# Kernel optimization log

Measured on AMD Instinct MI355X. Metric: run time of the kernel, lower is better.

The kernel has to match this reference:

```python
import jax, jax.numpy as jnp
import numpy as np

# Sparse 3D conv (stride-2 downsample) followed by the matching SparseInverseConv3d,
# implemented as rulebook-style gather-GEMM-scatter. Output coordinates of the
# inverse conv are exactly the input coordinates (spconv indice_key semantics).
SPATIAL = (41, 400, 352)          # (D, H, W) voxel grid
K, S, P, DIL = 3, 2, 1, 1          # kernel, stride, padding, dilation
IN_CH, OUT_CH = 32, 64
N_VOX = 120000
BATCH = 2

# static kernel offsets [27, 3]
OFFSETS = np.stack(np.meshgrid(np.arange(K), np.arange(K), np.arange(K), indexing='ij'), -1).reshape(-1, 3)
OUT_SHAPE = tuple((s + 2 * P - DIL * (K - 1) - 1) // S + 1 for s in SPATIAL)  # (21, 200, 176)


def setup_inputs() -> dict:
    key = jax.random.key(0)
    kf, kw1, kw2, kb, kz, ky, kx = jax.random.split(key, 7)
    features = jax.random.normal(kf, (N_VOX, IN_CH), jnp.float32)
    coors = jnp.stack([
        jax.random.randint(kb, (N_VOX,), 0, BATCH),
        jax.random.randint(kz, (N_VOX,), 0, SPATIAL[0]),
        jax.random.randint(ky, (N_VOX,), 0, SPATIAL[1]),
        jax.random.randint(kx, (N_VOX,), 0, SPATIAL[2]),
    ], axis=1).astype(jnp.int32)
    W1 = jax.random.normal(kw1, (K ** 3, IN_CH, OUT_CH), jnp.float32) * (1.0 / np.sqrt(K ** 3 * IN_CH))
    W2 = jax.random.normal(kw2, (K ** 3, OUT_CH, IN_CH), jnp.float32) * (1.0 / np.sqrt(K ** 3 * OUT_CH))
    return {"features": features, "coors": coors, "W1": W1, "W2": W2, "batch_size": BATCH}


def _rulebook(coors, batch_size):
    """Per kernel-offset linear output index + validity. lin == G marks invalid (dump slot)."""
    Dz, Hy, Wx = OUT_SHAPE
    G = batch_size * Dz * Hy * Wx
    b = coors[:, 0]
    c = coors[:, 1:]                                    # [N, 3]
    out_shape = jnp.asarray(OUT_SHAPE, jnp.int32)
    lins, valids = [], []
    for kv in range(K ** 3):
        off = jnp.asarray(OFFSETS[kv], jnp.int32)
        oc = c + P - DIL * off                          # numerator of output coord
        oq = oc // S
        valid = ((oc % S == 0) & (oq >= 0) & (oq < out_shape)).all(-1)
        lin = ((b * Dz + oq[:, 0]) * Hy + oq[:, 1]) * Wx + oq[:, 2]
        lins.append(jnp.where(valid, lin, G))
        valids.append(valid)
    return lins, G


def _spconv_forward(features, coors, W1, W2, batch_size):
    lins, G = _rulebook(coors, batch_size)
    # ---- SparseConv3d: gather(all inputs) -> GEMM per offset -> scatter-add to downsampled grid
    grid = jnp.zeros((G + 1, OUT_CH), features.dtype)   # last row = dump slot
    for kv in range(K ** 3):
        grid = grid.at[lins[kv]].add(features @ W1[kv])
    grid = grid.at[G].set(0.0)                          # clear dump slot -> invalid gathers read 0
    # ---- SparseInverseConv3d: transposed rulebook, output sites = original input coords
    out = jnp.zeros((features.shape[0], IN_CH), features.dtype)
    for kv in range(K ** 3):
        out = out + grid[lins[kv]] @ W2[kv]
    return out


def reference(features, coors, W1, W2, batch_size):
    return _spconv_forward(features, coors, W1, W2, int(batch_size))
```

## Files before the change

### kernel.cpp

```cpp
#include <hip/hip_runtime.h>
#include <stdint.h>


#define N_VOX 120000
#define IC 32
#define OC 64
#define NKV 27
#define DZ 21
#define HY 200
#define WX 176
#define TBL_BITS 20
#define TBL_SIZE (1 << TBL_BITS)
#define TBL_MASK (TBL_SIZE - 1)
#define MAXROWS 480000
#define VPW 128
#define VPBLK (VPW * 4)

#define OFF_KEYS 0
#define OFF_VALS 4194304
#define OFF_CNT 8388608
#define OFF_ROWS 8388864
#define OFF_FEATB 21348864
#define OFF_W2T 29028864
#define OFF_GRID 29139456
#define WS_NEEDED (OFF_GRID + (size_t)MAXROWS * OC * 2)

typedef __attribute__((ext_vector_type(8))) short short8;
typedef __attribute__((ext_vector_type(4))) float f32x4;

__device__ __forceinline__ uint32_t hash_lin(int lin) {
    return ((uint32_t)lin * 2654435761u) >> (32 - TBL_BITS);
}

__device__ __forceinline__ void atomAddF32(float* p, float v) {
    unsafeAtomicAdd(p, v);
}

__device__ __forceinline__ void atomPkBf16(uint16_t* p, uint32_t v) {
    asm volatile("global_atomic_pk_add_bf16 %0, %1, off" :: "v"(p), "v"(v) : "memory");
}

__device__ __forceinline__ uint32_t pk_bf16(float a, float b) {
    uint32_t x = __float_as_uint(a), y = __float_as_uint(b);
    x = (x + 0x7fffu + ((x >> 16) & 1u)) >> 16;
    y = (y + 0x7fffu + ((y >> 16) & 1u)) >> 16;
    return x | (y << 16);
}
__device__ __forceinline__ uint16_t f2bf(float a) {
    uint32_t x = __float_as_uint(a);
    return (uint16_t)((x + 0x7fffu + ((x >> 16) & 1u)) >> 16);
}

__device__ __forceinline__ float bf_lo(uint32_t u) { return __uint_as_float(u << 16); }
__device__ __forceinline__ float bf_hi(uint32_t u) { return __uint_as_float(u & 0xffff0000u); }

__global__ void k_init(int* keys, int* counter,
                       const float2* __restrict__ feat2, uint32_t* featb,
                       const float* __restrict__ W2, uint16_t* w2t) {
    int i = blockIdx.x * blockDim.x + threadIdx.x;
    int stride = gridDim.x * blockDim.x;
    for (int j = i; j < TBL_SIZE; j += stride) keys[j] = -1;
    for (int j = i; j < N_VOX * IC / 2; j += stride) {
        float2 f = feat2[j];
        featb[j] = pk_bf16(f.x, f.y);
    }
    for (int j = i; j < NKV * OC * IC; j += stride) {
        int kv = j >> 11, o = (j >> 5) & 63, c = j & 31;
        w2t[(kv << 11) + (c << 6) + o] = f2bf(W2[j]);
    }
    if (i == 0) *counter = 0;
}

__global__ void k_build(const int* __restrict__ coors, int* keys, int* rows) {
    int v = blockIdx.x * blockDim.x + threadIdx.x;
    if (v >= N_VOX) return;
    int b = coors[v * 4 + 0];
    int z = coors[v * 4 + 1];
    int y = coors[v * 4 + 2];
    int x = coors[v * 4 + 3];
#pragma unroll
    for (int kv = 0; kv < NKV; ++kv) {
        int oz = kv / 9, oy = (kv / 3) % 3, ox = kv % 3;
        int az = z + 1 - oz, ay = y + 1 - oy, ax = x + 1 - ox;
        int slot = -1;
        bool valid = (az >= 0) && !(az & 1) && ((az >> 1) < DZ) &&
                     (ay >= 0) && !(ay & 1) && ((ay >> 1) < HY) &&
                     (ax >= 0) && !(ax & 1) && ((ax >> 1) < WX);
        if (valid) {
            int lin = ((b * DZ + (az >> 1)) * HY + (ay >> 1)) * WX + (ax >> 1);
            uint32_t h = hash_lin(lin);
            for (;;) {
                int k = atomicCAS(&keys[h], -1, lin);
                if (k == -1 || k == lin) { slot = (int)h; break; }
                h = (h + 1) & TBL_MASK;
            }
        }
        rows[kv * N_VOX + v] = slot;
    }
}

__global__ __launch_bounds__(256) void k_assign(const int* __restrict__ keys,
                                                int* __restrict__ vals,
                                                int* counter,
                                                float4* __restrict__ grid4) {
    const int t = threadIdx.x;
    const int s0 = blockIdx.x * 2048 + t * 8;
    const int4 a = ((const int4*)(keys + s0))[0];
    const int4 b = ((const int4*)(keys + s0))[1];
    int k[8] = {a.x, a.y, a.z, a.w, b.x, b.y, b.z, b.w};
    int c = 0;
#pragma unroll
    for (int i = 0; i < 8; ++i) c += (k[i] != -1);

    __shared__ int sc[256];
    __shared__ int base;
    sc[t] = c;
    __syncthreads();
#pragma unroll
    for (int d = 1; d < 256; d <<= 1) {
        int y = (t >= d) ? sc[t - d] : 0;
        __syncthreads();
        sc[t] += y;
        __syncthreads();
    }
    if (t == 255) base = atomicAdd(counter, sc[255]);
    __syncthreads();
    const int total = sc[255];
    int r = base + sc[t] - c;
#pragma unroll
    for (int i = 0; i < 8; ++i) {
        if (k[i] != -1) { vals[s0 + i] = (r < MAXROWS) ? r : -1; ++r; }
    }
    int zs = min(base, MAXROWS), ze = min(base + total, MAXROWS);
    float4 zz = {0.f, 0.f, 0.f, 0.f};
    for (int i = zs * 8 + t; i < ze * 8; i += 256) grid4[i] = zz;
}

__global__ void k_rows_fix(int* rows, const int* __restrict__ vals) {
    int i = blockIdx.x * blockDim.x + threadIdx.x;
    if (i >= NKV * N_VOX) return;
    int s = rows[i];
    rows[i] = (s >= 0) ? vals[s] : -1;
}

__device__ __forceinline__ int compact_pairs(const int* __restrict__ rkv,
                                             int v0, int lane, int2* ls) {
    int n = 0;
#pragma unroll
    for (int ch = 0; ch < VPW / 64; ++ch) {
        int v = v0 + ch * 64 + lane;
        int row = (v < N_VOX) ? rkv[v] : -1;
        unsigned long long m = __ballot(row >= 0);
        int pos = n + (int)__popcll(m & ((1ULL << lane) - 1));
        if (row >= 0) ls[pos] = make_int2(v, row);
        n += (int)__popcll(m);
    }
    return n;
}

__global__ __launch_bounds__(256, 8) void k_scatter(
    const uint4* __restrict__ featb, const float* __restrict__ W1,
    const int* __restrict__ rows, uint16_t* gridb) {
    const int kv = blockIdx.y;
    const int wid = threadIdx.x >> 6;
    const int lane = threadIdx.x & 63;
    __shared__ int2 ls[4][VPW];

    float w[IC];
#pragma unroll
    for (int c = 0; c < IC; ++c) w[c] = W1[(kv * IC + c) * OC + lane];

    const int v0 = (blockIdx.x * 4 + wid) * VPW;
    const int n = (v0 < N_VOX)
                      ? compact_pairs(rows + kv * N_VOX, v0, lane, ls[wid])
                      : 0;

    for (int p = 0; p < n; p += 2) {
        const bool hasB = (p + 1 < n);
        const int2 A = ls[wid][p];
        const int2 B = ls[wid][hasB ? p + 1 : p];
        const uint4* pA = featb + A.x * 4;
        const uint4* pB = featb + B.x * 4;
        uint4 fA[4], fB[4];
#pragma unroll
        for (int j = 0; j < 4; ++j) { fA[j] = pA[j]; fB[j] = pB[j]; }
        float accA = 0.f, accB = 0.f;
#pragma unroll
        for (int j = 0; j < 4; ++j) {
            const uint32_t ua[4] = {fA[j].x, fA[j].y, fA[j].z, fA[j].w};
            const uint32_t ub[4] = {fB[j].x, fB[j].y, fB[j].z, fB[j].w};
#pragma unroll
            for (int m = 0; m < 4; ++m) {
                const int cb = j * 8 + m * 2;
                accA = fmaf(bf_lo(ua[m]), w[cb + 0], accA);
                accA = fmaf(bf_hi(ua[m]), w[cb + 1], accA);
                accB = fmaf(bf_lo(ub[m]), w[cb + 0], accB);
                accB = fmaf(bf_hi(ub[m]), w[cb + 1], accB);
            }
        }
        float oA = __shfl_xor(accA, 1, 64);
        float oB = __shfl_xor(accB, 1, 64);
        if ((lane & 1) == 0) {
            atomPkBf16(gridb + (size_t)A.y * OC + lane, pk_bf16(accA, oA));
            if (hasB) atomPkBf16(gridb + (size_t)B.y * OC + lane, pk_bf16(accB, oB));
        }
    }
}

__global__ __launch_bounds__(256) void k_gather_v(
    const uint16_t* __restrict__ gridb, const uint16_t* __restrict__ w2t,
    const int* __restrict__ rows, float* __restrict__ out) {
    const int wid = threadIdx.x >> 6;
    const int lane = threadIdx.x & 63;
    const int v0 = (blockIdx.x * 4 + wid) * 32;
    if (v0 >= N_VOX) return;
    const int lg = lane >> 4;
    const int li = lane & 15;

    f32x4 acc[2][2] = {{{0.f, 0.f, 0.f, 0.f}, {0.f, 0.f, 0.f, 0.f}},
                       {{0.f, 0.f, 0.f, 0.f}, {0.f, 0.f, 0.f, 0.f}}};

    for (int kv = 0; kv < NKV; ++kv) {
        const int* rkv = rows + kv * N_VOX;
        const uint16_t* w2k = w2t + ((size_t)kv << 11);
        short8 b[2][2];
#pragma unroll
        for (int nt = 0; nt < 2; ++nt)
#pragma unroll
            for (int kh = 0; kh < 2; ++kh)
                b[nt][kh] = *(const short8*)(w2k + (nt * 16 + li) * 64 +
                                             kh * 32 + lg * 8);
#pragma unroll
        for (int mt = 0; mt < 2; ++mt) {
            const int v = v0 + mt * 16 + li;
            const int r = (v < N_VOX) ? rkv[v] : -1;
            short8 a0 = {0, 0, 0, 0, 0, 0, 0, 0};
            short8 a1 = {0, 0, 0, 0, 0, 0, 0, 0};
            if (r >= 0) {
                const uint16_t* gr = gridb + (size_t)r * OC;
                a0 = *(const short8*)(gr + lg * 8);
                a1 = *(const short8*)(gr + 32 + lg * 8);
            }
            acc[mt][0] = __builtin_amdgcn_mfma_f32_16x16x32_bf16(a0, b[0][0], acc[mt][0], 0, 0, 0);
            acc[mt][0] = __builtin_amdgcn_mfma_f32_16x16x32_bf16(a1, b[0][1], acc[mt][0], 0, 0, 0);
            acc[mt][1] = __builtin_amdgcn_mfma_f32_16x16x32_bf16(a0, b[1][0], acc[mt][1], 0, 0, 0);
            acc[mt][1] = __builtin_amdgcn_mfma_f32_16x16x32_bf16(a1, b[1][1], acc[mt][1], 0, 0, 0);
        }
    }
#pragma unroll
    for (int mt = 0; mt < 2; ++mt)
#pragma unroll
        for (int nt = 0; nt < 2; ++nt)
#pragma unroll
            for (int rg = 0; rg < 4; ++rg) {
                const int v = v0 + mt * 16 + lg * 4 + rg;
                if (v < N_VOX) out[(size_t)v * IC + nt * 16 + li] = acc[mt][nt][rg];
            }
}

extern "C" void kernel_launch(void* const* d_in, const int* in_sizes, int n_in,
                              void* d_out, int out_size, void* d_ws, size_t ws_size,
                              hipStream_t stream) {
    const float* feat = (const float*)d_in[0];
    const int* coors = (const int*)d_in[1];
    const float* W1 = (const float*)d_in[2];
    const float* W2 = (const float*)d_in[3];
    float* out = (float*)d_out;

    if (ws_size < WS_NEEDED) return;

    char* ws = (char*)d_ws;
    int* keys = (int*)(ws + OFF_KEYS);
    int* vals = (int*)(ws + OFF_VALS);
    int* counter = (int*)(ws + OFF_CNT);
    int* rows = (int*)(ws + OFF_ROWS);
    uint32_t* featb = (uint32_t*)(ws + OFF_FEATB);
    uint16_t* w2t = (uint16_t*)(ws + OFF_W2T);
    uint16_t* gridb = (uint16_t*)(ws + OFF_GRID);

    k_init<<<dim3(4096), dim3(256), 0, stream>>>(keys, counter,
                                                 (const float2*)feat, featb,
                                                 W2, w2t);
    k_build<<<dim3((N_VOX + 255) / 256), dim3(256), 0, stream>>>(coors, keys, rows);
    k_assign<<<dim3(TBL_SIZE / 2048), dim3(256), 0, stream>>>(keys, vals, counter,
                                                              (float4*)gridb);
    k_rows_fix<<<dim3((NKV * N_VOX + 255) / 256), dim3(256), 0, stream>>>(rows, vals);

    dim3 gs((N_VOX + VPBLK - 1) / VPBLK, NKV);
    k_scatter<<<gs, dim3(256), 0, stream>>>((const uint4*)featb, W1, rows, gridb);

    k_gather_v<<<dim3((N_VOX + 127) / 128), dim3(256), 0, stream>>>(gridb, w2t,
                                                                    rows, out);
}
```

Measured before the change: 280.8 us.

## Rewrite forward scatter as MFMA GEMM over 32-voxel tiles with bf16 W1

The per-offset scalar FMA scatter kernel, with its ballot compaction, is replaced by a wave-level kernel. It loads 32 voxels' bf16 features once and, for each of the 27 offsets, computes a 32x64 tile with bf16 MFMA before atomically adding packed bf16 pairs into the grid. W1 is now pre-converted to transposed bf16 in the init kernel. Bounds checks on N_VOX are removed because N_VOX is a multiple of 32. This cuts FMA instruction count and repeated feature loads, but it now does MFMA work for invalid rows and issues atomics in a scattered pattern with shuffles per element.

```diff
diff --git a/kernel.cpp b/kernel.cpp
--- a/kernel.cpp
+++ b/kernel.cpp
@@ -13,8 +13,6 @@
 #define TBL_SIZE (1 << TBL_BITS)
 #define TBL_MASK (TBL_SIZE - 1)
 #define MAXROWS 480000
-#define VPW 128
-#define VPBLK (VPW * 4)
 
 #define OFF_KEYS 0
 #define OFF_VALS 4194304
@@ -22,7 +20,8 @@
 #define OFF_ROWS 8388864
 #define OFF_FEATB 21348864
 #define OFF_W2T 29028864
-#define OFF_GRID 29139456
+#define OFF_W1T 29139456
+#define OFF_GRID 29250048
 #define WS_NEEDED (OFF_GRID + (size_t)MAXROWS * OC * 2)
 
 typedef __attribute__((ext_vector_type(8))) short short8;
@@ -30,10 +29,6 @@
 
 __device__ __forceinline__ uint32_t hash_lin(int lin) {
     return ((uint32_t)lin * 2654435761u) >> (32 - TBL_BITS);
-}
-
-__device__ __forceinline__ void atomAddF32(float* p, float v) {
-    unsafeAtomicAdd(p, v);
 }
 
 __device__ __forceinline__ void atomPkBf16(uint16_t* p, uint32_t v) {
@@ -51,11 +46,9 @@
     return (uint16_t)((x + 0x7fffu + ((x >> 16) & 1u)) >> 16);
 }
 
-__device__ __forceinline__ float bf_lo(uint32_t u) { return __uint_as_float(u << 16); }
-__device__ __forceinline__ float bf_hi(uint32_t u) { return __uint_as_float(u & 0xffff0000u); }
-
 __global__ void k_init(int* keys, int* counter,
                        const float2* __restrict__ feat2, uint32_t* featb,
+                       const float* __restrict__ W1, uint16_t* w1t,
                        const float* __restrict__ W2, uint16_t* w2t) {
     int i = blockIdx.x * blockDim.x + threadIdx.x;
     int stride = gridDim.x * blockDim.x;
@@ -63,6 +56,10 @@
     for (int j = i; j < N_VOX * IC / 2; j += stride) {
         float2 f = feat2[j];
         featb[j] = pk_bf16(f.x, f.y);
+    }
+    for (int j = i; j < NKV * IC * OC; j += stride) {
+        int kv = j >> 11, c = (j >> 6) & 31, o = j & 63;
+        w1t[(kv << 11) + (o << 5) + c] = f2bf(W1[j]);
     }
     for (int j = i; j < NKV * OC * IC; j += stride) {
         int kv = j >> 11, o = (j >> 5) & 63, c = j & 31;
@@ -143,66 +140,48 @@
     rows[i] = (s >= 0) ? vals[s] : -1;
 }
 
-__device__ __forceinline__ int compact_pairs(const int* __restrict__ rkv,
-                                             int v0, int lane, int2* ls) {
-    int n = 0;
-#pragma unroll
-    for (int ch = 0; ch < VPW / 64; ++ch) {
-        int v = v0 + ch * 64 + lane;
-        int row = (v < N_VOX) ? rkv[v] : -1;
-        unsigned long long m = __ballot(row >= 0);
-        int pos = n + (int)__popcll(m & ((1ULL << lane) - 1));
-        if (row >= 0) ls[pos] = make_int2(v, row);
-        n += (int)__popcll(m);
-    }
-    return n;
-}
-
-__global__ __launch_bounds__(256, 8) void k_scatter(
-    const uint4* __restrict__ featb, const float* __restrict__ W1,
+__global__ __launch_bounds__(256) void k_scatter_v(
+    const uint16_t* __restrict__ featb, const uint16_t* __restrict__ w1t,
     const int* __restrict__ rows, uint16_t* gridb) {
-    const int kv = blockIdx.y;
     const int wid = threadIdx.x >> 6;
     const int lane = threadIdx.x & 63;
-    __shared__ int2 ls[4][VPW];
-
-    float w[IC];
-#pragma unroll
-    for (int c = 0; c < IC; ++c) w[c] = W1[(kv * IC + c) * OC + lane];
-
-    const int v0 = (blockIdx.x * 4 + wid) * VPW;
-    const int n = (v0 < N_VOX)
-                      ? compact_pairs(rows + kv * N_VOX, v0, lane, ls[wid])
-                      : 0;
-
-    for (int p = 0; p < n; p += 2) {
-        const bool hasB = (p + 1 < n);
-        const int2 A = ls[wid][p];
-        const int2 B = ls[wid][hasB ? p + 1 : p];
-        const uint4* pA = featb + A.x * 4;
-        const uint4* pB = featb + B.x * 4;
-        uint4 fA[4], fB[4];
-#pragma unroll
-        for (int j = 0; j < 4; ++j) { fA[j] = pA[j]; fB[j] = pB[j]; }
-        float accA = 0.f, accB = 0.f;
-#pragma unroll
-        for (int j = 0; j < 4; ++j) {
-            const uint32_t ua[4] = {fA[j].x, fA[j].y, fA[j].z, fA[j].w};
-            const uint32_t ub[4] = {fB[j].x, fB[j].y, fB[j].z, fB[j].w};
-#pragma unroll
-            for (int m = 0; m < 4; ++m) {
-                const int cb = j * 8 + m * 2;
-                accA = fmaf(bf_lo(ua[m]), w[cb + 0], accA);
-                accA = fmaf(bf_hi(ua[m]), w[cb + 1], accA);
-                accB = fmaf(bf_lo(ub[m]), w[cb + 0], accB);
-                accB = fmaf(bf_hi(ub[m]), w[cb + 1], accB);
-            }
-        }
-        float oA = __shfl_xor(accA, 1, 64);
-        float oB = __shfl_xor(accB, 1, 64);
-        if ((lane & 1) == 0) {
-            atomPkBf16(gridb + (size_t)A.y * OC + lane, pk_bf16(accA, oA));
-            if (hasB) atomPkBf16(gridb + (size_t)B.y * OC + lane, pk_bf16(accB, oB));
+    const int v0 = (blockIdx.x * 4 + wid) * 32;
+    if (v0 >= N_VOX) return;
+    const int lg = lane >> 4;
+    const int li = lane & 15;
+
+    short8 a[2];
+#pragma unroll
+    for (int mt = 0; mt < 2; ++mt)
+        a[mt] = *(const short8*)(featb + (size_t)(v0 + mt * 16 + li) * IC + lg * 8);
+
+    for (int kv = 0; kv < NKV; ++kv) {
+        const int* rkv = rows + kv * N_VOX;
+        const uint16_t* w1k = w1t + (kv << 11);
+        short8 b[4];
+#pragma unroll
+        for (int nt = 0; nt < 4; ++nt)
+            b[nt] = *(const short8*)(w1k + (nt * 16 + li) * IC + lg * 8);
+        int4 r4[2];
+#pragma unroll
+        for (int mt = 0; mt < 2; ++mt)
+            r4[mt] = *(const int4*)(rkv + v0 + mt * 16 + lg * 4);
+#pragma unroll
+        for (int mt = 0; mt < 2; ++mt) {
+            const int rr[4] = {r4[mt].x, r4[mt].y, r4[mt].z, r4[mt].w};
+#pragma unroll
+            for (int nt = 0; nt < 4; ++nt) {
+                f32x4 d = {0.f, 0.f, 0.f, 0.f};
+                d = __builtin_amdgcn_mfma_f32_16x16x32_bf16(a[mt], b[nt], d, 0, 0, 0);
+#pragma unroll
+                for (int rg = 0; rg < 4; ++rg) {
+                    float other = __shfl_xor(d[rg], 1, 64);
+                    if ((li & 1) == 0 && rr[rg] >= 0) {
+                        atomPkBf16(gridb + (size_t)rr[rg] * OC + nt * 16 + li,
+                                   pk_bf16(d[rg], other));
+                    }
+                }
+            }
         }
     }
 }
@@ -233,7 +212,7 @@
 #pragma unroll
         for (int mt = 0; mt < 2; ++mt) {
             const int v = v0 + mt * 16 + li;
-            const int r = (v < N_VOX) ? rkv[v] : -1;
+            const int r = rkv[v];
             short8 a0 = {0, 0, 0, 0, 0, 0, 0, 0};
             short8 a1 = {0, 0, 0, 0, 0, 0, 0, 0};
             if (r >= 0) {
@@ -254,7 +233,7 @@
 #pragma unroll
             for (int rg = 0; rg < 4; ++rg) {
                 const int v = v0 + mt * 16 + lg * 4 + rg;
-                if (v < N_VOX) out[(size_t)v * IC + nt * 16 + li] = acc[mt][nt][rg];
+                out[(size_t)v * IC + nt * 16 + li] = acc[mt][nt][rg];
             }
 }
 
@@ -276,19 +255,19 @@
     int* rows = (int*)(ws + OFF_ROWS);
     uint32_t* featb = (uint32_t*)(ws + OFF_FEATB);
     uint16_t* w2t = (uint16_t*)(ws + OFF_W2T);
+    uint16_t* w1t = (uint16_t*)(ws + OFF_W1T);
     uint16_t* gridb = (uint16_t*)(ws + OFF_GRID);
 
     k_init<<<dim3(4096), dim3(256), 0, stream>>>(keys, counter,
                                                  (const float2*)feat, featb,
-                                                 W2, w2t);
+                                                 W1, w1t, W2, w2t);
     k_build<<<dim3((N_VOX + 255) / 256), dim3(256), 0, stream>>>(coors, keys, rows);
     k_assign<<<dim3(TBL_SIZE / 2048), dim3(256), 0, stream>>>(keys, vals, counter,
                                                               (float4*)gridb);
     k_rows_fix<<<dim3((NKV * N_VOX + 255) / 256), dim3(256), 0, stream>>>(rows, vals);
 
-    dim3 gs((N_VOX + VPBLK - 1) / VPBLK, NKV);
-    k_scatter<<<gs, dim3(256), 0, stream>>>((const uint4*)featb, W1, rows, gridb);
-
-    k_gather_v<<<dim3((N_VOX + 127) / 128), dim3(256), 0, stream>>>(gridb, w2t,
-                                                                    rows, out);
-}
+    const int nblk = (N_VOX + 127) / 128;
+    k_scatter_v<<<dim3(nblk), dim3(256), 0, stream>>>((const uint16_t*)featb,
+                                                      w1t, rows, gridb);
+    k_gather_v<<<dim3(nblk), dim3(256), 0, stream>>>(gridb, w2t, rows, out);
+}
```

Result: faster. 226.6 us (-19.3%).
